# Kernel optimization log

Measured on AMD Instinct MI355X. Metric: run time of the kernel, lower is better.

## Reference

```python
import jax, jax.numpy as jnp
import numpy as np

B, T, C, H = 8, 4096, 1024, 128  # batch, seq, n_embd, head_size


def setup_inputs() -> dict:
    key = jax.random.key(0)
    ks = jax.random.split(key, 4)
    std = 1.0 / np.sqrt(C)
    return {
        "x": jax.random.normal(ks[0], (B, T, C), dtype=jnp.float32),
        "Wq": jax.random.normal(ks[1], (C, H), dtype=jnp.float32) * std,
        "bq": jnp.zeros((H,), dtype=jnp.float32),
        "Wk": jax.random.normal(ks[2], (C, H), dtype=jnp.float32) * std,
        "bk": jnp.zeros((H,), dtype=jnp.float32),
        "Wv": jax.random.normal(ks[3], (C, H), dtype=jnp.float32) * std,
        "bv": jnp.zeros((H,), dtype=jnp.float32),
    }


def reference(x, Wq, bq, Wk, bk, Wv, bv):
    # Q, K, V projections: [B, T, H]
    q = x @ Wq + bq
    k = x @ Wk + bk
    v = x @ Wv + bv
    scale = jnp.asarray(H, x.dtype) ** -0.5
    # scaled attention scores: [B, T, T]
    wei = jnp.einsum("bqh,bkh->bqk", q, k) * scale
    # causal mask: position q attends to k <= q
    causal = jnp.tril(jnp.ones((T, T), dtype=bool))
    wei = jnp.where(causal[None, :, :], wei, jnp.finfo(x.dtype).min)
    wei = jax.nn.softmax(wei, axis=-1)
    # dropout p=0.0 (eval) -> identity
    out = jnp.einsum("bqk,bkh->bqh", wei, v)  # [B, T, H]
    return out
```

## Files before the change

### kernel.cpp

```cpp
#include <hip/hip_runtime.h>
#include <hip/hip_bf16.h>

typedef __attribute__((ext_vector_type(8))) short short8;
typedef __attribute__((ext_vector_type(4))) short shortx4;
typedef __attribute__((ext_vector_type(4))) float floatx4;
typedef __attribute__((ext_vector_type(4))) unsigned int uintx4;

#define BB 8
#define TT 4096
#define CC 1024
#define HH 128
#define BT (BB * TT)
#define MBASE 16.0f

__device__ __forceinline__ unsigned short f2bf(float f) {
    unsigned int u = __float_as_uint(f);
    u += 0x7fffu + ((u >> 16) & 1u);
    return (unsigned short)(u >> 16);
}

__device__ __forceinline__ void async16(const unsigned short* g, unsigned short* l) {
    __builtin_amdgcn_global_load_lds(
        (const __attribute__((address_space(1))) unsigned int*)g,
        (__attribute__((address_space(3))) unsigned int*)l, 16, 0, 0);
}

__global__ void conv_w(const float* __restrict__ Wq, const float* __restrict__ Wk,
                       const float* __restrict__ Wv, unsigned short* __restrict__ Wt) {
    __shared__ float tile[32][33];
    const int w = blockIdx.z, nt = blockIdx.y, kt = blockIdx.x;
    const int tx = threadIdx.x, ty = threadIdx.y;
    const float* W = (w == 0) ? Wq : ((w == 1) ? Wk : Wv);
#pragma unroll
    for (int i = 0; i < 4; ++i)
        tile[ty + 8 * i][tx] = W[(kt * 32 + ty + 8 * i) * HH + nt * 32 + tx];
    __syncthreads();
#pragma unroll
    for (int i = 0; i < 4; ++i)
        Wt[w * (HH * CC) + (nt * 32 + ty + 8 * i) * CC + kt * 32 + tx] = f2bf(tile[tx][ty + 8 * i]);
}

__global__ __launch_bounds__(512, 4) void proj_gemm(
    const float* __restrict__ x, const unsigned short* __restrict__ Wt,
    const float* __restrict__ bq, const float* __restrict__ bk, const float* __restrict__ bv,
    unsigned short* __restrict__ Qb, unsigned short* __restrict__ Kb,
    unsigned short* __restrict__ Vt) {
    __shared__ unsigned short Bs[3][192 * 64];
    const int gid = blockIdx.x;
    const int c = gid & 7, j = gid >> 3;
    const int mb = c * 32 + (j >> 1);
    const int nb = j & 1;
    const int tid = threadIdx.x, lane = tid & 63, wv = tid >> 6;
    const int quad = lane >> 4, l15 = lane & 15;
    const int brow = lane >> 3;
    const int wc = (lane & 7) ^ (brow & 7);
    const unsigned short* Wp = Wt + (long)nb * 192 * CC;
    const float* xw = x + ((long)mb * 128 + wv * 16 + l15) * CC + quad * 8;
    const int rw = mb * 128 + wv * 16;

    floatx4 acc[12];
#pragma unroll
    for (int jj = 0; jj < 12; ++jj) {
        floatx4 z = {0.f, 0.f, 0.f, 0.f};
        acc[jj] = z;
    }

    floatx4 pf[4];
    short8 af[2];

    auto loadA = [&](int kt) {
#pragma unroll
        for (int ks = 0; ks < 2; ++ks) {
            const float* p = xw + kt * 64 + ks * 32;
            pf[ks * 2]     = *(const floatx4*)p;
            pf[ks * 2 + 1] = *(const floatx4*)(p + 4);
        }
    };
    auto cvtA = [&]() {
#pragma unroll
        for (int ks = 0; ks < 2; ++ks) {
            floatx4 a = pf[ks * 2], b2 = pf[ks * 2 + 1];
            short8 r;
            r[0] = (short)f2bf(a[0]);  r[1] = (short)f2bf(a[1]);
            r[2] = (short)f2bf(a[2]);  r[3] = (short)f2bf(a[3]);
            r[4] = (short)f2bf(b2[0]); r[5] = (short)f2bf(b2[1]);
            r[6] = (short)f2bf(b2[2]); r[7] = (short)f2bf(b2[3]);
            af[ks] = r;
        }
    };
    auto stageB = [&](int kt, int buf) {
#pragma unroll
        for (int h = 0; h < 3; ++h) {
            int grp = 8 * h + wv;
            async16(Wp + (long)(grp * 8 + brow) * CC + kt * 64 + wc * 8, &Bs[buf][grp * 512]);
        }
    };

    loadA(0);
    stageB(0, 0);
    stageB(1, 1);
    __builtin_amdgcn_sched_barrier(0);
    asm volatile("s_waitcnt vmcnt(3)" ::: "memory");
    __builtin_amdgcn_s_barrier();
    __builtin_amdgcn_sched_barrier(0);
    int cur = 0;

    for (int kt = 0; kt < 16; ++kt) {
        cvtA();
        if (kt < 15) loadA(kt + 1);
        __builtin_amdgcn_sched_barrier(0);
        if (kt < 14) {
            int b2 = cur ? cur - 1 : 2;
            stageB(kt + 2, b2);
        }
        __builtin_amdgcn_sched_barrier(0);

        const unsigned short* Bc = Bs[cur];
#pragma unroll
        for (int ks = 0; ks < 2; ++ks)
#pragma unroll
            for (int ni = 0; ni < 12; ++ni) {
                short8 bfr = *(const short8*)&Bc[(ni * 16 + l15) * 64 +
                                                 (((ks * 4 + quad) ^ (l15 & 7)) * 8)];
                acc[ni] = __builtin_amdgcn_mfma_f32_16x16x32_bf16(af[ks], bfr, acc[ni], 0, 0, 0);
            }
        __builtin_amdgcn_sched_barrier(0);

        if (kt < 15) {
            if (kt < 14) { asm volatile("s_waitcnt vmcnt(7)" ::: "memory"); }
            else         { asm volatile("s_waitcnt vmcnt(4)" ::: "memory"); }
            __builtin_amdgcn_s_barrier();
            __builtin_amdgcn_sched_barrier(0);
            cur = (cur == 2) ? 0 : cur + 1;
        }
    }

    const float qscale = 0.08838834764831845f * 1.4426950408889634f;
    unsigned short* Tw = &Bs[1][wv * 768];
#pragma unroll
    for (int ni = 0; ni < 12; ++ni) {
        int f = 12 * nb + ni;
        int col = f * 16 + l15;
        int h = col & 127;
        if (f < 16) {
            float bval = (f < 8) ? bq[h] : bk[h];
            unsigned short* dst = (f < 8) ? Qb : Kb;
#pragma unroll
            for (int r = 0; r < 4; ++r) {
                int row = rw + quad * 4 + r;
                float v = acc[ni][r] + bval;
                if (f < 8) v *= qscale;
                dst[(long)row * HH + h] = f2bf(v);
            }
        } else {
            float bval = bv[h];
            shortx4 pk;
#pragma unroll
            for (int r = 0; r < 4; ++r) pk[r] = (short)f2bf(acc[ni][r] + bval);
            *(shortx4*)&Tw[l15 * 48 + quad * 4] = pk;
            if (lane < 32) {
                int th = lane >> 1, seg = lane & 1;
                uintx4 q0 = *(const uintx4*)&Tw[th * 48 + seg * 8];
                int hg = (f - 16) * 16 + th;
                int bb = rw >> 12, t0 = (rw & 4095) + seg * 8;
                unsigned short* vp = Vt + (long)bb * (HH * TT) + (long)hg * TT + t0;
                *(uintx4*)vp = q0;
            }
        }
    }
}

__global__ __launch_bounds__(512, 2) void attn(
    const unsigned short* __restrict__ Qb, const unsigned short* __restrict__ Kb,
    const unsigned short* __restrict__ Vt, unsigned short* __restrict__ Op,
    float* __restrict__ Lh) {
    __shared__ unsigned short Ks[64 * 128];
    __shared__ unsigned short Vs[128 * 64];
    __shared__ unsigned short Ps[8 * 16 * 40];
    const int gid = blockIdx.x;
    const int b = gid & 7;
    const int idx = gid >> 3;
    const int qp = idx >> 2;
    const int s = idx & 3;
    const int qb0 = 62 - 2 * qp;
    const int len2 = qb0 + 2;
    const int lo = (s * len2) >> 2;
    const int hi = ((s + 1) * len2) >> 2;
    const int tid = threadIdx.x, lane = tid & 63, wv = tid >> 6;
    const int quad = lane >> 4, l15 = lane & 15;
    const int qb_w = qb0 + (wv >> 2);
    const int hi_eff = (hi < qb_w + 1) ? hi : qb_w + 1;

    short8 qf[4];
    {
        const unsigned short* qp_ = Qb + ((long)b * TT + qb0 * 64 + wv * 16 + l15) * HH + quad * 8;
#pragma unroll
        for (int ks = 0; ks < 4; ++ks) qf[ks] = *(const short8*)(qp_ + ks * 32);
    }
    floatx4 o[8];
#pragma unroll
    for (int i = 0; i < 8; ++i) {
        floatx4 z = {0.f, 0.f, 0.f, 0.f};
        o[i] = z;
    }
    float l_part[4] = {0.f, 0.f, 0.f, 0.f};

    const int kc = l15 ^ ((4 * wv + quad) & 15);
    const unsigned short* Kg = Kb + (long)b * TT * HH + ((long)lo * 64 + 4 * wv + quad) * HH + kc * 8;
    const int vrow = lane >> 3;
    const int vc = (lane & 7) ^ vrow;
    const unsigned short* Vg = Vt + (long)b * HH * TT + (long)(8 * wv + vrow) * TT + lo * 64 + vc * 8;
    unsigned short* Pw = &Ps[wv * 640];

    for (int kb = lo; kb < hi; ++kb) {
#pragma unroll
        for (int h = 0; h < 2; ++h) {
            int grp = 8 * h + wv;
            async16(Kg + (long)h * 32 * HH, &Ks[grp * 512]);
            async16(Vg + (long)h * 64 * TT, &Vs[grp * 512]);
        }
        Kg += (long)64 * HH;
        Vg += 64;
        __syncthreads();

        if (kb <= qb_w) {
            floatx4 sArr[4];
#pragma unroll
            for (int nt = 0; nt < 4; ++nt) {
                floatx4 z = {0.f, 0.f, 0.f, 0.f};
                sArr[nt] = z;
            }
            __builtin_amdgcn_s_setprio(1);
#pragma unroll
            for (int ks = 0; ks < 4; ++ks)
#pragma unroll
                for (int nt = 0; nt < 4; ++nt) {
                    short8 kf = *(const short8*)&Ks[(nt * 16 + l15) * 128 + (((ks * 4 + quad) ^ l15) * 8)];
                    sArr[nt] = __builtin_amdgcn_mfma_f32_16x16x32_bf16(qf[ks], kf, sArr[nt], 0, 0, 0);
                }
            __builtin_amdgcn_s_setprio(0);

            if (kb == qb_w) {
                int rowl = (wv & 3) * 16 + quad * 4;
#pragma unroll
                for (int nt = 0; nt < 4; ++nt) {
                    int col = nt * 16 + l15;
#pragma unroll
                    for (int r = 0; r < 4; ++r)
                        if (col > rowl + r) sArr[nt][r] = -1e30f;
                }
            }

#pragma unroll
            for (int nt = 0; nt < 4; ++nt)
#pragma unroll
                for (int r = 0; r < 4; ++r)
                    sArr[nt][r] = exp2f(sArr[nt][r] - MBASE);
#pragma unroll
            for (int r = 0; r < 4; ++r)
                l_part[r] += (sArr[0][r] + sArr[1][r]) + (sArr[2][r] + sArr[3][r]);

#pragma unroll
            for (int k2 = 0; k2 < 2; ++k2) {
#pragma unroll
                for (int ntl = 0; ntl < 2; ++ntl)
#pragma unroll
                    for (int r = 0; r < 4; ++r)
                        Pw[(quad * 4 + r) * 40 + ntl * 16 + l15] = f2bf(sArr[k2 * 2 + ntl][r]);
                short8 pfrag = *(const short8*)&Pw[l15 * 40 + quad * 8];
                __builtin_amdgcn_s_setprio(1);
#pragma unroll
                for (int hn = 0; hn < 8; ++hn) {
                    short8 vf = *(const short8*)&Vs[(hn * 16 + l15) * 64 +
                                                    (((k2 * 4 + quad) ^ (l15 & 7)) * 8)];
                    o[hn] = __builtin_amdgcn_mfma_f32_16x16x32_bf16(pfrag, vf, o[hn], 0, 0, 0);
                }
                __builtin_amdgcn_s_setprio(0);
            }
        }
        __syncthreads();
    }

    long rbase = (long)b * TT + qb0 * 64 + wv * 16 + quad * 4;
    unsigned short* Os = Op + (long)s * BT * HH;
    if (hi_eff > lo) {
#pragma unroll
        for (int hn = 0; hn < 8; ++hn)
#pragma unroll
            for (int r = 0; r < 4; ++r)
                Os[(rbase + r) * HH + hn * 16 + l15] = f2bf(o[hn][r]);
    }
#pragma unroll
    for (int r = 0; r < 4; ++r) {
        float l = l_part[r];
#pragma unroll
        for (int off = 1; off < 16; off <<= 1) l += __shfl_xor(l, off);
        if (l15 == 0) Lh[(long)s * BT + rbase + r] = (hi_eff > lo) ? l : 0.f;
    }
}

__global__ __launch_bounds__(256) void merge_kern(
    const unsigned short* __restrict__ Op, const float* __restrict__ Lh,
    float* __restrict__ out) {
    long e = ((long)blockIdx.x * 256 + threadIdx.x) * 8;
    long row = e >> 7;
    float lsum = Lh[row] + Lh[BT + row] + Lh[2 * (long)BT + row] + Lh[3 * (long)BT + row];
    float inv = 1.f / lsum;
    float acc[8];
#pragma unroll
    for (int j = 0; j < 8; ++j) acc[j] = 0.f;
#pragma unroll
    for (int s = 0; s < 4; ++s) {
        float ls = Lh[(long)s * BT + row];
        if (ls > 0.f) {
            uintx4 p = *(const uintx4*)(Op + (long)s * BT * HH + e);
#pragma unroll
            for (int j = 0; j < 4; ++j) {
                acc[2 * j]     += __uint_as_float(p[j] << 16);
                acc[2 * j + 1] += __uint_as_float(p[j] & 0xffff0000u);
            }
        }
    }
    floatx4 o0, o1;
#pragma unroll
    for (int j = 0; j < 4; ++j) {
        if (j < 2) { o0[2 * j] = acc[2 * j] * inv; o0[2 * j + 1] = acc[2 * j + 1] * inv; }
        else { o1[2 * (j - 2)] = acc[2 * j] * inv; o1[2 * (j - 2) + 1] = acc[2 * j + 1] * inv; }
    }
    *(floatx4*)(out + e) = o0;
    *(floatx4*)(out + e + 4) = o1;
}

extern "C" void kernel_launch(void* const* d_in, const int* in_sizes, int n_in,
                              void* d_out, int out_size, void* d_ws, size_t ws_size,
                              hipStream_t stream) {
    const float* x  = (const float*)d_in[0];
    const float* Wq = (const float*)d_in[1];
    const float* bq = (const float*)d_in[2];
    const float* Wk = (const float*)d_in[3];
    const float* bk = (const float*)d_in[4];
    const float* Wv = (const float*)d_in[5];
    const float* bv = (const float*)d_in[6];
    float* out = (float*)d_out;

    char* ws = (char*)d_ws;
    unsigned short* Wt = (unsigned short*)(ws);
    unsigned short* Qb = (unsigned short*)(ws + 1048576);
    unsigned short* Kb = (unsigned short*)(ws + 9437184);
    unsigned short* Vt = (unsigned short*)(ws + 17825792);
    unsigned short* Op = (unsigned short*)(ws + 26214400);
    float*          Lh = (float*)(ws + 59768832);

    conv_w<<<dim3(32, 4, 3), dim3(32, 8), 0, stream>>>(Wq, Wk, Wv, Wt);
    proj_gemm<<<512, 512, 0, stream>>>(x, Wt, bq, bk, bv, Qb, Kb, Vt);
    attn<<<1024, 512, 0, stream>>>(Qb, Kb, Vt, Op, Lh);
    merge_kern<<<2048, 256, 0, stream>>>(Op, Lh, out);
}
```

Baseline: 290.6 us.

## Prefetch next K/V tile into registers and raise attention occupancy

Replaces the direct global-to-LDS async loads with register-staged loads, where the next K/V tile is issued right after the barrier so its global latency overlaps the current tile's MFMA work. Launch bounds change from 2 to 4 blocks per CU to allow more waves. The cost is extra VGPRs for the staging registers alongside the tighter register cap, which risks spills. It also adds explicit waitcnt, barrier and sched_barrier sequencing that replaces __syncthreads.

Measured after the change: 292.5 us. Within noise of the previous version (+0.7%).

```diff
diff --git a/kernel.cpp b/kernel.cpp
--- a/kernel.cpp
+++ b/kernel.cpp
@@ -170,7 +170,7 @@
     }
 }
 
-__global__ __launch_bounds__(512, 2) void attn(
+__global__ __launch_bounds__(512, 4) void attn(
     const unsigned short* __restrict__ Qb, const unsigned short* __restrict__ Kb,
     const unsigned short* __restrict__ Vt, unsigned short* __restrict__ Op,
     float* __restrict__ Lh) {
@@ -210,18 +210,34 @@
     const int vrow = lane >> 3;
     const int vc = (lane & 7) ^ vrow;
     const unsigned short* Vg = Vt + (long)b * HH * TT + (long)(8 * wv + vrow) * TT + lo * 64 + vc * 8;
+    unsigned short* KsW0 = &Ks[(unsigned)wv * 512 + (unsigned)lane * 8];
+    unsigned short* KsW1 = &Ks[(unsigned)(8 + wv) * 512 + (unsigned)lane * 8];
+    unsigned short* VsW0 = &Vs[(unsigned)wv * 512 + (unsigned)lane * 8];
+    unsigned short* VsW1 = &Vs[(unsigned)(8 + wv) * 512 + (unsigned)lane * 8];
     unsigned short* Pw = &Ps[wv * 640];
 
-    for (int kb = lo; kb < hi; ++kb) {
-#pragma unroll
-        for (int h = 0; h < 2; ++h) {
-            int grp = 8 * h + wv;
-            async16(Kg + (long)h * 32 * HH, &Ks[grp * 512]);
-            async16(Vg + (long)h * 64 * TT, &Vs[grp * 512]);
-        }
+    uintx4 kr0, kr1, vr0, vr1;
+    auto issueKV = [&]() {
+        kr0 = *(const uintx4*)(Kg);
+        kr1 = *(const uintx4*)(Kg + 32 * HH);
+        vr0 = *(const uintx4*)(Vg);
+        vr1 = *(const uintx4*)(Vg + (long)64 * TT);
         Kg += (long)64 * HH;
         Vg += 64;
-        __syncthreads();
+    };
+
+    issueKV();
+
+    for (int kb = lo; kb < hi; ++kb) {
+        asm volatile("s_waitcnt vmcnt(0)" ::: "memory");
+        *(uintx4*)KsW0 = kr0;
+        *(uintx4*)KsW1 = kr1;
+        *(uintx4*)VsW0 = vr0;
+        *(uintx4*)VsW1 = vr1;
+        asm volatile("s_waitcnt lgkmcnt(0)" ::: "memory");
+        __builtin_amdgcn_s_barrier();
+        if (kb + 1 < hi) issueKV();
+        __builtin_amdgcn_sched_barrier(0);
 
         if (kb <= qb_w) {
             floatx4 sArr[4];
@@ -278,7 +294,7 @@
                 __builtin_amdgcn_s_setprio(0);
             }
         }
-        __syncthreads();
+        __builtin_amdgcn_s_barrier();
     }
 
     long rbase = (long)b * TT + qb0 * 64 + wv * 16 + quad * 4;
```

## Halve attention block to 4 waves, each computing 32 query rows

Applied to the files above, without the earlier changes.

The attention kernel drops from 8 waves of 16 query rows to 4 waves of 32 query rows per block, so each wave processes two M-tiles. Each K and V fragment read from LDS is reused across both tiles, which halves LDS read traffic per MFMA. Each thread now issues twice as many async loads per tile. The cost is higher register pressure (double the accumulators and score tiles) and fewer waves per CU to hide latency.

Measured after the change: 293.0 us. Within noise of the previous version (+0.8%).

```diff
diff --git a/kernel.cpp b/kernel.cpp
--- a/kernel.cpp
+++ b/kernel.cpp
@@ -170,13 +170,13 @@
     }
 }
 
-__global__ __launch_bounds__(512, 2) void attn(
+__global__ __launch_bounds__(256, 2) void attn(
     const unsigned short* __restrict__ Qb, const unsigned short* __restrict__ Kb,
     const unsigned short* __restrict__ Vt, unsigned short* __restrict__ Op,
     float* __restrict__ Lh) {
     __shared__ unsigned short Ks[64 * 128];
     __shared__ unsigned short Vs[128 * 64];
-    __shared__ unsigned short Ps[8 * 16 * 40];
+    __shared__ unsigned short Ps[4 * 2 * 16 * 40];
     const int gid = blockIdx.x;
     const int b = gid & 7;
     const int idx = gid >> 3;
@@ -188,92 +188,113 @@
     const int hi = ((s + 1) * len2) >> 2;
     const int tid = threadIdx.x, lane = tid & 63, wv = tid >> 6;
     const int quad = lane >> 4, l15 = lane & 15;
-    const int qb_w = qb0 + (wv >> 2);
+    const int qb_w = qb0 + (wv >> 1);
     const int hi_eff = (hi < qb_w + 1) ? hi : qb_w + 1;
-
-    short8 qf[4];
+    const int rw = qb0 * 64 + wv * 32;
+
+    short8 qf[2][4];
     {
-        const unsigned short* qp_ = Qb + ((long)b * TT + qb0 * 64 + wv * 16 + l15) * HH + quad * 8;
-#pragma unroll
-        for (int ks = 0; ks < 4; ++ks) qf[ks] = *(const short8*)(qp_ + ks * 32);
-    }
-    floatx4 o[8];
-#pragma unroll
-    for (int i = 0; i < 8; ++i) {
-        floatx4 z = {0.f, 0.f, 0.f, 0.f};
-        o[i] = z;
-    }
-    float l_part[4] = {0.f, 0.f, 0.f, 0.f};
-
-    const int kc = l15 ^ ((4 * wv + quad) & 15);
+        const unsigned short* qp_ = Qb + ((long)b * TT + rw + l15) * HH + quad * 8;
+#pragma unroll
+        for (int mi = 0; mi < 2; ++mi)
+#pragma unroll
+            for (int ks = 0; ks < 4; ++ks)
+                qf[mi][ks] = *(const short8*)(qp_ + (long)mi * 16 * HH + ks * 32);
+    }
+    floatx4 o[2][8];
+#pragma unroll
+    for (int mi = 0; mi < 2; ++mi)
+#pragma unroll
+        for (int i = 0; i < 8; ++i) {
+            floatx4 z = {0.f, 0.f, 0.f, 0.f};
+            o[mi][i] = z;
+        }
+    float l_part[2][4] = {{0.f, 0.f, 0.f, 0.f}, {0.f, 0.f, 0.f, 0.f}};
+
+    const int kc = l15 ^ (4 * wv + quad);
     const unsigned short* Kg = Kb + (long)b * TT * HH + ((long)lo * 64 + 4 * wv + quad) * HH + kc * 8;
     const int vrow = lane >> 3;
-    const int vc = (lane & 7) ^ vrow;
+    const int vc = (lane & 7) ^ (vrow & 7);
     const unsigned short* Vg = Vt + (long)b * HH * TT + (long)(8 * wv + vrow) * TT + lo * 64 + vc * 8;
-    unsigned short* Pw = &Ps[wv * 640];
+    unsigned short* Pw = &Ps[wv * 1280];
 
     for (int kb = lo; kb < hi; ++kb) {
 #pragma unroll
-        for (int h = 0; h < 2; ++h) {
-            int grp = 8 * h + wv;
-            async16(Kg + (long)h * 32 * HH, &Ks[grp * 512]);
-            async16(Vg + (long)h * 64 * TT, &Vs[grp * 512]);
+        for (int h = 0; h < 4; ++h) {
+            int grp = 4 * h + wv;
+            async16(Kg + (long)h * (16 * HH), &Ks[grp * 512]);
+            async16(Vg + (long)h * 32 * TT, &Vs[grp * 512]);
         }
         Kg += (long)64 * HH;
         Vg += 64;
         __syncthreads();
 
         if (kb <= qb_w) {
-            floatx4 sArr[4];
-#pragma unroll
-            for (int nt = 0; nt < 4; ++nt) {
-                floatx4 z = {0.f, 0.f, 0.f, 0.f};
-                sArr[nt] = z;
-            }
+            floatx4 sArr[2][4];
+#pragma unroll
+            for (int mi = 0; mi < 2; ++mi)
+#pragma unroll
+                for (int nt = 0; nt < 4; ++nt) {
+                    floatx4 z = {0.f, 0.f, 0.f, 0.f};
+                    sArr[mi][nt] = z;
+                }
             __builtin_amdgcn_s_setprio(1);
 #pragma unroll
             for (int ks = 0; ks < 4; ++ks)
 #pragma unroll
                 for (int nt = 0; nt < 4; ++nt) {
                     short8 kf = *(const short8*)&Ks[(nt * 16 + l15) * 128 + (((ks * 4 + quad) ^ l15) * 8)];
-                    sArr[nt] = __builtin_amdgcn_mfma_f32_16x16x32_bf16(qf[ks], kf, sArr[nt], 0, 0, 0);
+                    sArr[0][nt] = __builtin_amdgcn_mfma_f32_16x16x32_bf16(qf[0][ks], kf, sArr[0][nt], 0, 0, 0);
+                    sArr[1][nt] = __builtin_amdgcn_mfma_f32_16x16x32_bf16(qf[1][ks], kf, sArr[1][nt], 0, 0, 0);
                 }
             __builtin_amdgcn_s_setprio(0);
 
             if (kb == qb_w) {
-                int rowl = (wv & 3) * 16 + quad * 4;
-#pragma unroll
-                for (int nt = 0; nt < 4; ++nt) {
-                    int col = nt * 16 + l15;
+                int rbt = (wv & 1) * 32;
+#pragma unroll
+                for (int mi = 0; mi < 2; ++mi) {
+                    int rowl = rbt + mi * 16 + quad * 4;
+#pragma unroll
+                    for (int nt = 0; nt < 4; ++nt) {
+                        int col = nt * 16 + l15;
+#pragma unroll
+                        for (int r = 0; r < 4; ++r)
+                            if (col > rowl + r) sArr[mi][nt][r] = -1e30f;
+                    }
+                }
+            }
+
+#pragma unroll
+            for (int mi = 0; mi < 2; ++mi) {
+#pragma unroll
+                for (int nt = 0; nt < 4; ++nt)
 #pragma unroll
                     for (int r = 0; r < 4; ++r)
-                        if (col > rowl + r) sArr[nt][r] = -1e30f;
-                }
-            }
-
-#pragma unroll
-            for (int nt = 0; nt < 4; ++nt)
+                        sArr[mi][nt][r] = exp2f(sArr[mi][nt][r] - MBASE);
 #pragma unroll
                 for (int r = 0; r < 4; ++r)
-                    sArr[nt][r] = exp2f(sArr[nt][r] - MBASE);
-#pragma unroll
-            for (int r = 0; r < 4; ++r)
-                l_part[r] += (sArr[0][r] + sArr[1][r]) + (sArr[2][r] + sArr[3][r]);
+                    l_part[mi][r] += (sArr[mi][0][r] + sArr[mi][1][r]) + (sArr[mi][2][r] + sArr[mi][3][r]);
+            }
 
 #pragma unroll
             for (int k2 = 0; k2 < 2; ++k2) {
 #pragma unroll
-                for (int ntl = 0; ntl < 2; ++ntl)
-#pragma unroll
-                    for (int r = 0; r < 4; ++r)
-                        Pw[(quad * 4 + r) * 40 + ntl * 16 + l15] = f2bf(sArr[k2 * 2 + ntl][r]);
-                short8 pfrag = *(const short8*)&Pw[l15 * 40 + quad * 8];
+                for (int mi = 0; mi < 2; ++mi)
+#pragma unroll
+                    for (int ntl = 0; ntl < 2; ++ntl)
+#pragma unroll
+                        for (int r = 0; r < 4; ++r)
+                            Pw[mi * 640 + (quad * 4 + r) * 40 + ntl * 16 + l15] =
+                                f2bf(sArr[mi][k2 * 2 + ntl][r]);
+                short8 pf0 = *(const short8*)&Pw[l15 * 40 + quad * 8];
+                short8 pf1 = *(const short8*)&Pw[640 + l15 * 40 + quad * 8];
                 __builtin_amdgcn_s_setprio(1);
 #pragma unroll
                 for (int hn = 0; hn < 8; ++hn) {
                     short8 vf = *(const short8*)&Vs[(hn * 16 + l15) * 64 +
                                                     (((k2 * 4 + quad) ^ (l15 & 7)) * 8)];
-                    o[hn] = __builtin_amdgcn_mfma_f32_16x16x32_bf16(pfrag, vf, o[hn], 0, 0, 0);
+                    o[0][hn] = __builtin_amdgcn_mfma_f32_16x16x32_bf16(pf0, vf, o[0][hn], 0, 0, 0);
+                    o[1][hn] = __builtin_amdgcn_mfma_f32_16x16x32_bf16(pf1, vf, o[1][hn], 0, 0, 0);
                 }
                 __builtin_amdgcn_s_setprio(0);
             }
@@ -281,21 +302,24 @@
         __syncthreads();
     }
 
-    long rbase = (long)b * TT + qb0 * 64 + wv * 16 + quad * 4;
     unsigned short* Os = Op + (long)s * BT * HH;
-    if (hi_eff > lo) {
-#pragma unroll
-        for (int hn = 0; hn < 8; ++hn)
-#pragma unroll
-            for (int r = 0; r < 4; ++r)
-                Os[(rbase + r) * HH + hn * 16 + l15] = f2bf(o[hn][r]);
-    }
-#pragma unroll
-    for (int r = 0; r < 4; ++r) {
-        float l = l_part[r];
-#pragma unroll
-        for (int off = 1; off < 16; off <<= 1) l += __shfl_xor(l, off);
-        if (l15 == 0) Lh[(long)s * BT + rbase + r] = (hi_eff > lo) ? l : 0.f;
+#pragma unroll
+    for (int mi = 0; mi < 2; ++mi) {
+        long rbase = (long)b * TT + rw + mi * 16 + quad * 4;
+        if (hi_eff > lo) {
+#pragma unroll
+            for (int hn = 0; hn < 8; ++hn)
+#pragma unroll
+                for (int r = 0; r < 4; ++r)
+                    Os[(rbase + r) * HH + hn * 16 + l15] = f2bf(o[mi][hn][r]);
+        }
+#pragma unroll
+        for (int r = 0; r < 4; ++r) {
+            float l = l_part[mi][r];
+#pragma unroll
+            for (int off = 1; off < 16; off <<= 1) l += __shfl_xor(l, off);
+            if (l15 == 0) Lh[(long)s * BT + rbase + r] = (hi_eff > lo) ? l : 0.f;
+        }
     }
 }
 
@@ -353,6 +377,6 @@
 
     conv_w<<<dim3(32, 4, 3), dim3(32, 8), 0, stream>>>(Wq, Wk, Wv, Wt);
     proj_gemm<<<512, 512, 0, stream>>>(x, Wt, bq, bk, bv, Qb, Kb, Vt);
-    attn<<<1024, 512, 0, stream>>>(Qb, Kb, Vt, Op, Lh);
+    attn<<<1024, 256, 0, stream>>>(Qb, Kb, Vt, Op, Lh);
     merge_kern<<<2048, 256, 0, stream>>>(Op, Lh, out);
 }
```
